# Performance work log

Hardware: AMD Instinct MI355X
Metric: run time of the kernel (lower is better)

## Reference

```python
import jax, jax.numpy as jnp
import numpy as np
import math

B, T, C = 32768, 32, 32  # seq len and embed dim are pinned to 32 by the source code


def setup_inputs() -> dict:
    key = jax.random.key(0)
    ks = jax.random.split(key, 9)
    s = 1.0 / math.sqrt(C)
    x = jax.random.normal(ks[0], (B, T, C), jnp.float32)
    Wk = jax.random.normal(ks[1], (C, C), jnp.float32) * s
    bk = jax.random.normal(ks[2], (C,), jnp.float32) * s
    Wq = jax.random.normal(ks[3], (C, C), jnp.float32) * s
    bq = jax.random.normal(ks[4], (C,), jnp.float32) * s
    Wv = jax.random.normal(ks[5], (C, C), jnp.float32) * s
    bv = jax.random.normal(ks[6], (C,), jnp.float32) * s
    Wp = jax.random.normal(ks[7], (C, C), jnp.float32) * s
    bp = jax.random.normal(ks[8], (C,), jnp.float32) * s
    return {"x": x, "Wk": Wk, "bk": bk, "Wq": Wq, "bq": bq,
            "Wv": Wv, "bv": bv, "Wp": Wp, "bp": bp}


def reference(x, Wk, bk, Wq, bq, Wv, bv, Wp, bp):
    # torch Linear: y = x @ W^T + b
    k = x @ Wk.T + bk          # [B, T, C]
    q = x @ Wq.T + bq
    v = x @ Wv.T + bv
    # att = q k^T / sqrt(C)  -> [B, T, T]
    att = jnp.matmul(q, jnp.swapaxes(k, -2, -1)) / math.sqrt(C)
    # mask is [1,1,T,T]; out-of-place masked_fill broadcasts att to [1,B,T,T]
    mask = jnp.tril(jnp.ones((T, T), jnp.float32))[None, None]  # [1,1,T,T]
    att = jnp.where(mask == 0, -jnp.inf, att[None])             # [1,B,T,T]
    att = jax.nn.softmax(att, axis=-1)
    # y = att @ v^T : [1,B,T,T] @ [B,C,T] -> [1,B,T,T]  (valid because C == T)
    y = jnp.matmul(att, jnp.swapaxes(v, -2, -1))
    # transpose(1,2) then view(B, -1, C) -- faithful permutation + reshape
    y = jnp.transpose(y, (0, 2, 1, 3)).reshape(B, -1, C)        # [B, T, C]
    return y @ Wp.T + bp
```

## Files before the change

### kernel.cpp

```cpp
#include <hip/hip_runtime.h>

typedef __bf16 bf16x8 __attribute__((ext_vector_type(8)));
typedef float  f32x16 __attribute__((ext_vector_type(16)));

static_assert(sizeof(bf16x8) == 16, "bf16x8 must be 16B");

#define MFMA32(A, B, C) __builtin_amdgcn_mfma_f32_32x32x16_bf16((A), (B), (C), 0, 0, 0)

__device__ __forceinline__ bf16x8 load8_bf(const float* __restrict__ p, float scale) {
    const float4 a = *reinterpret_cast<const float4*>(p);
    const float4 b = *reinterpret_cast<const float4*>(p + 4);
    bf16x8 r;
    r[0] = (__bf16)(a.x * scale); r[1] = (__bf16)(a.y * scale);
    r[2] = (__bf16)(a.z * scale); r[3] = (__bf16)(a.w * scale);
    r[4] = (__bf16)(b.x * scale); r[5] = (__bf16)(b.y * scale);
    r[6] = (__bf16)(b.z * scale); r[7] = (__bf16)(b.w * scale);
    return r;
}

__device__ __forceinline__ unsigned short f2bf(float f) {
    return __builtin_bit_cast(unsigned short, (__bf16)f);
}

__device__ __forceinline__ f32x16 zero16() {
    f32x16 z;
#pragma unroll
    for (int e = 0; e < 16; ++e) z[e] = 0.f;
    return z;
}


__global__ __launch_bounds__(256) void attn32(
    const float* __restrict__ x,
    const float* __restrict__ Wk, const float* __restrict__ bk,
    const float* __restrict__ Wq, const float* __restrict__ bq,
    const float* __restrict__ Wv, const float* __restrict__ bv,
    const float* __restrict__ Wp, const float* __restrict__ bp,
    float* __restrict__ out, int Btot)
{
    __shared__ float4 lds4[4][480];

    const int lane = threadIdx.x & 63;
    const int wave = threadIdx.x >> 6;
    const int col  = lane & 31;
    const int hi   = lane >> 5;

    char* const base = (char*)lds4[wave];
    unsigned short* const qk16 = (unsigned short*)base;
    unsigned short* const v16  = (unsigned short*)(base + 5120);

    const float RS32 = 0.17677669529663687f;

    const int wrow = col * 32 + hi * 8;
    const bf16x8 wk0 = load8_bf(Wk + wrow, 1.f), wk1 = load8_bf(Wk + wrow + 16, 1.f);
    const bf16x8 wq0 = load8_bf(Wq + wrow, RS32), wq1 = load8_bf(Wq + wrow + 16, RS32);
    const bf16x8 wv0 = load8_bf(Wv + wrow, 1.f), wv1 = load8_bf(Wv + wrow + 16, 1.f);
    const bf16x8 wp0 = load8_bf(Wp + wrow, 1.f), wp1 = load8_bf(Wp + wrow + 16, 1.f);
    const float bkv = bk[col];
    const float bqv = bq[col] * RS32;
    const float bvv = bv[col];
    const float bpv = bp[col];

    const int gw = blockIdx.x * (blockDim.x >> 6) + wave;
    const int nw = gridDim.x * (blockDim.x >> 6);

    for (int b = gw; b < Btot; b += nw) {
        const float* xb = x + (size_t)b * 1024;

        const bf16x8 xa0 = load8_bf(xb + col * 32 + hi * 8, 1.f);
        const bf16x8 xa1 = load8_bf(xb + col * 32 + 16 + hi * 8, 1.f);

        f32x16 acc;

        acc = zero16();
        acc = MFMA32(xa0, wk0, acc);
        acc = MFMA32(xa1, wk1, acc);
#pragma unroll
        for (int e = 0; e < 16; ++e) {
            const int r = (e & 3) + 8 * (e >> 2) + 4 * hi;
            qk16[1280 + r * 40 + col] = f2bf(acc[e] + bkv);
        }
        acc = zero16();
        acc = MFMA32(xa0, wq0, acc);
        acc = MFMA32(xa1, wq1, acc);
#pragma unroll
        for (int e = 0; e < 16; ++e) {
            const int r = (e & 3) + 8 * (e >> 2) + 4 * hi;
            qk16[r * 40 + col] = f2bf(acc[e] + bqv);
        }
        acc = zero16();
        acc = MFMA32(xa0, wv0, acc);
        acc = MFMA32(xa1, wv1, acc);
#pragma unroll
        for (int e = 0; e < 16; ++e) {
            const int r = (e & 3) + 8 * (e >> 2) + 4 * hi;
            v16[r * 40 + col] = f2bf(acc[e] + bvv);
        }

        asm volatile("" ::: "memory");

        const bf16x8 qa0 = *(const bf16x8*)(base + col * 80 + hi * 16);
        const bf16x8 qa1 = *(const bf16x8*)(base + col * 80 + 32 + hi * 16);
        const bf16x8 kb0 = *(const bf16x8*)(base + 2560 + col * 80 + hi * 16);
        const bf16x8 kb1 = *(const bf16x8*)(base + 2560 + col * 80 + 32 + hi * 16);
        acc = zero16();
        acc = MFMA32(qa0, kb0, acc);
        acc = MFMA32(qa1, kb1, acc);

        float* const sf = (float*)base;
#pragma unroll
        for (int e = 0; e < 16; ++e) {
            const int r = (e & 3) + 8 * (e >> 2) + 4 * hi;
            sf[r * 36 + col] = acc[e];
        }

        asm volatile("" ::: "memory");

        float sv[16];
        {
            const char* sb = base + col * 144 + hi * 32;
            *(float4*)&sv[0]  = *(const float4*)(sb);
            *(float4*)&sv[4]  = *(const float4*)(sb + 16);
            *(float4*)&sv[8]  = *(const float4*)(sb + 64);
            *(float4*)&sv[12] = *(const float4*)(sb + 80);
        }
        const int i = col;
#pragma unroll
        for (int e = 0; e < 16; ++e) {
            const int j = (e < 8) ? (hi * 8 + e) : (16 + hi * 8 + (e - 8));
            if (j > i) sv[e] = -__builtin_inff();
        }
        float m = sv[0];
#pragma unroll
        for (int e = 1; e < 16; ++e) m = fmaxf(m, sv[e]);
        m = fmaxf(m, __shfl_xor(m, 32));
        float pe[16];
        float sum = 0.f;
#pragma unroll
        for (int e = 0; e < 16; ++e) { pe[e] = __expf(sv[e] - m); sum += pe[e]; }
        sum += __shfl_xor(sum, 32);
        const float inv = 1.f / sum;
        bf16x8 p0, p1;
#pragma unroll
        for (int e = 0; e < 8; ++e) {
            p0[e] = (__bf16)(pe[e] * inv);
            p1[e] = (__bf16)(pe[8 + e] * inv);
        }

        const bf16x8 vb0 = *(const bf16x8*)(base + 5120 + col * 80 + hi * 16);
        const bf16x8 vb1 = *(const bf16x8*)(base + 5120 + col * 80 + 32 + hi * 16);
        acc = zero16();
        acc = MFMA32(p0, vb0, acc);
        acc = MFMA32(p1, vb1, acc);

#pragma unroll
        for (int e = 0; e < 16; ++e) {
            const int r = (e & 3) + 8 * (e >> 2) + 4 * hi;
            qk16[r * 40 + col] = f2bf(acc[e]);
        }

        asm volatile("" ::: "memory");

        const bf16x8 ya0 = *(const bf16x8*)(base + col * 80 + hi * 16);
        const bf16x8 ya1 = *(const bf16x8*)(base + col * 80 + 32 + hi * 16);
        acc = zero16();
        acc = MFMA32(ya0, wp0, acc);
        acc = MFMA32(ya1, wp1, acc);

        float* const ob = out + (size_t)b * 32 + col;
#pragma unroll
        for (int e = 0; e < 16; ++e) {
            const int r = (e & 3) + 8 * (e >> 2) + 4 * hi;
            ob[(size_t)r << 20] = acc[e] + bpv;
        }

        asm volatile("" ::: "memory");
    }
}

extern "C" void kernel_launch(void* const* d_in, const int* in_sizes, int n_in,
                              void* d_out, int out_size, void* d_ws, size_t ws_size,
                              hipStream_t stream) {
    const float* x  = (const float*)d_in[0];
    const float* Wk = (const float*)d_in[1];
    const float* bk = (const float*)d_in[2];
    const float* Wq = (const float*)d_in[3];
    const float* bq = (const float*)d_in[4];
    const float* Wv = (const float*)d_in[5];
    const float* bv = (const float*)d_in[6];
    const float* Wp = (const float*)d_in[7];
    const float* bp = (const float*)d_in[8];
    float* out = (float*)d_out;

    const int Btot = in_sizes[0] / 1024;
    dim3 grid(2048), block(256);
    hipLaunchKernelGGL(attn32, grid, block, 0, stream,
                       x, Wk, bk, Wq, bq, Wv, bv, Wp, bp, out, Btot);
}
```

Before: 60.42 us.

## Keep attention intermediates in registers via permlane32 swaps instead of LDS

Computes transposed products (W·x^T, K·Q^T, V·P^T) so each MFMA output can be repacked into the next MFMA's operand layout with bf16 packing and v_permlane32_swap, removing all LDS round-trips for Q, K, V, scores and Y. Biases are folded into the accumulator init, softmax uses exp2 with log2e folded into the Q scale plus a fast reciprocal, and the next batch's x is prefetched into registers. Output stores become nontemporal and launch bounds request 3 blocks per CU. This raises register pressure and relies on the permlane32_swap intrinsic or inline asm being available.

```diff
diff --git a/kernel.cpp b/kernel.cpp
--- a/kernel.cpp
+++ b/kernel.cpp
@@ -2,8 +2,7 @@
 
 typedef __bf16 bf16x8 __attribute__((ext_vector_type(8)));
 typedef float  f32x16 __attribute__((ext_vector_type(16)));
-
-static_assert(sizeof(bf16x8) == 16, "bf16x8 must be 16B");
+typedef unsigned int uint4v __attribute__((ext_vector_type(4)));
 
 #define MFMA32(A, B, C) __builtin_amdgcn_mfma_f32_32x32x16_bf16((A), (B), (C), 0, 0, 0)
 
@@ -18,19 +17,45 @@
     return r;
 }
 
-__device__ __forceinline__ unsigned short f2bf(float f) {
-    return __builtin_bit_cast(unsigned short, (__bf16)f);
+__device__ __forceinline__ unsigned pack2(float a, float b) {
+    unsigned la = (unsigned)__builtin_bit_cast(unsigned short, (__bf16)a);
+    unsigned lb = (unsigned)__builtin_bit_cast(unsigned short, (__bf16)b);
+    return la | (lb << 16);
 }
 
-__device__ __forceinline__ f32x16 zero16() {
-    f32x16 z;
-#pragma unroll
-    for (int e = 0; e < 16; ++e) z[e] = 0.f;
-    return z;
+__device__ __forceinline__ void swap32(unsigned& a, unsigned& b) {
+#if __has_builtin(__builtin_amdgcn_permlane32_swap)
+    auto r = __builtin_amdgcn_permlane32_swap(a, b, false, false);
+    a = r[0]; b = r[1];
+#else
+    asm("v_permlane32_swap_b32 %0, %1" : "+v"(a), "+v"(b));
+#endif
 }
 
+__device__ __forceinline__ void rearrange(const f32x16& a, bf16x8& f0, bf16x8& f1) {
+    unsigned D0 = pack2(a[0], a[1]),   D1 = pack2(a[2], a[3]);
+    unsigned D2 = pack2(a[4], a[5]),   D3 = pack2(a[6], a[7]);
+    unsigned D4 = pack2(a[8], a[9]),   D5 = pack2(a[10], a[11]);
+    unsigned D6 = pack2(a[12], a[13]), D7 = pack2(a[14], a[15]);
+    swap32(D0, D2); swap32(D1, D3); swap32(D4, D6); swap32(D5, D7);
+    f0 = __builtin_bit_cast(bf16x8, uint4v{D0, D1, D2, D3});
+    f1 = __builtin_bit_cast(bf16x8, uint4v{D4, D5, D6, D7});
+}
 
-__global__ __launch_bounds__(256) void attn32(
+__device__ __forceinline__ void ld4(const float* __restrict__ p,
+                                    float4& r0, float4& r1, float4& r2, float4& r3) {
+    r0 = *reinterpret_cast<const float4*>(p);
+    r1 = *reinterpret_cast<const float4*>(p + 4);
+    r2 = *reinterpret_cast<const float4*>(p + 16);
+    r3 = *reinterpret_cast<const float4*>(p + 20);
+}
+
+__device__ __forceinline__ void cvt8(const float4& a, const float4& b, bf16x8& f) {
+    f[0] = (__bf16)a.x; f[1] = (__bf16)a.y; f[2] = (__bf16)a.z; f[3] = (__bf16)a.w;
+    f[4] = (__bf16)b.x; f[5] = (__bf16)b.y; f[6] = (__bf16)b.z; f[7] = (__bf16)b.w;
+}
+
+__global__ __launch_bounds__(256, 3) void attn32(
     const float* __restrict__ x,
     const float* __restrict__ Wk, const float* __restrict__ bk,
     const float* __restrict__ Wq, const float* __restrict__ bq,
@@ -38,143 +63,103 @@
     const float* __restrict__ Wp, const float* __restrict__ bp,
     float* __restrict__ out, int Btot)
 {
-    __shared__ float4 lds4[4][480];
-
     const int lane = threadIdx.x & 63;
-    const int wave = threadIdx.x >> 6;
     const int col  = lane & 31;
     const int hi   = lane >> 5;
 
-    char* const base = (char*)lds4[wave];
-    unsigned short* const qk16 = (unsigned short*)base;
-    unsigned short* const v16  = (unsigned short*)(base + 5120);
-
-    const float RS32 = 0.17677669529663687f;
+    const float SC = 0.17677669529663687f * 1.4426950408889634f;
 
     const int wrow = col * 32 + hi * 8;
     const bf16x8 wk0 = load8_bf(Wk + wrow, 1.f), wk1 = load8_bf(Wk + wrow + 16, 1.f);
-    const bf16x8 wq0 = load8_bf(Wq + wrow, RS32), wq1 = load8_bf(Wq + wrow + 16, RS32);
+    const bf16x8 wq0 = load8_bf(Wq + wrow, SC),  wq1 = load8_bf(Wq + wrow + 16, SC);
     const bf16x8 wv0 = load8_bf(Wv + wrow, 1.f), wv1 = load8_bf(Wv + wrow + 16, 1.f);
     const bf16x8 wp0 = load8_bf(Wp + wrow, 1.f), wp1 = load8_bf(Wp + wrow + 16, 1.f);
-    const float bkv = bk[col];
-    const float bqv = bq[col] * RS32;
-    const float bvv = bv[col];
+
+    f32x16 bk16, bq16, bv16;
+#pragma unroll
+    for (int e = 0; e < 16; ++e) {
+        const int r = (e & 3) + 8 * (e >> 2) + 4 * hi;
+        bk16[e] = bk[r];
+        bq16[e] = bq[r] * SC;
+        bv16[e] = bv[r];
+    }
     const float bpv = bp[col];
 
-    const int gw = blockIdx.x * (blockDim.x >> 6) + wave;
-    const int nw = gridDim.x * (blockDim.x >> 6);
+    const int gw = blockIdx.x * 4 + (threadIdx.x >> 6);
+    const int nw = gridDim.x * 4;
+
+    float4 A0, A1, A2, A3;
+    if (gw < Btot) ld4(x + (size_t)gw * 1024 + wrow, A0, A1, A2, A3);
 
     for (int b = gw; b < Btot; b += nw) {
-        const float* xb = x + (size_t)b * 1024;
-
-        const bf16x8 xa0 = load8_bf(xb + col * 32 + hi * 8, 1.f);
-        const bf16x8 xa1 = load8_bf(xb + col * 32 + 16 + hi * 8, 1.f);
+        bf16x8 xa0, xa1;
+        cvt8(A0, A1, xa0);
+        cvt8(A2, A3, xa1);
+        const int nb = b + nw;
+        if (nb < Btot) ld4(x + (size_t)nb * 1024 + wrow, A0, A1, A2, A3);
 
         f32x16 acc;
 
-        acc = zero16();
-        acc = MFMA32(xa0, wk0, acc);
-        acc = MFMA32(xa1, wk1, acc);
+        acc = bk16;
+        acc = MFMA32(wk0, xa0, acc);
+        acc = MFMA32(wk1, xa1, acc);
+        bf16x8 ka0, ka1; rearrange(acc, ka0, ka1);
+
+        acc = bq16;
+        acc = MFMA32(wq0, xa0, acc);
+        acc = MFMA32(wq1, xa1, acc);
+        bf16x8 qb0, qb1; rearrange(acc, qb0, qb1);
+
+        acc = bv16;
+        acc = MFMA32(wv0, xa0, acc);
+        acc = MFMA32(wv1, xa1, acc);
+        bf16x8 vb0, vb1; rearrange(acc, vb0, vb1);
+
+        f32x16 s;
+#pragma unroll
+        for (int e = 0; e < 16; ++e) s[e] = 0.f;
+        s = MFMA32(ka0, qb0, s);
+        s = MFMA32(ka1, qb1, s);
+
+        float sv[16];
+        float m = -3.0e38f;
 #pragma unroll
         for (int e = 0; e < 16; ++e) {
-            const int r = (e & 3) + 8 * (e >> 2) + 4 * hi;
-            qk16[1280 + r * 40 + col] = f2bf(acc[e] + bkv);
+            const int j = (e & 3) + 8 * (e >> 2) + 4 * hi;
+            sv[e] = (j <= col) ? s[e] : -__builtin_inff();
+            m = fmaxf(m, sv[e]);
         }
-        acc = zero16();
-        acc = MFMA32(xa0, wq0, acc);
-        acc = MFMA32(xa1, wq1, acc);
-#pragma unroll
-        for (int e = 0; e < 16; ++e) {
-            const int r = (e & 3) + 8 * (e >> 2) + 4 * hi;
-            qk16[r * 40 + col] = f2bf(acc[e] + bqv);
-        }
-        acc = zero16();
-        acc = MFMA32(xa0, wv0, acc);
-        acc = MFMA32(xa1, wv1, acc);
-#pragma unroll
-        for (int e = 0; e < 16; ++e) {
-            const int r = (e & 3) + 8 * (e >> 2) + 4 * hi;
-            v16[r * 40 + col] = f2bf(acc[e] + bvv);
-        }
-
-        asm volatile("" ::: "memory");
-
-        const bf16x8 qa0 = *(const bf16x8*)(base + col * 80 + hi * 16);
-        const bf16x8 qa1 = *(const bf16x8*)(base + col * 80 + 32 + hi * 16);
-        const bf16x8 kb0 = *(const bf16x8*)(base + 2560 + col * 80 + hi * 16);
-        const bf16x8 kb1 = *(const bf16x8*)(base + 2560 + col * 80 + 32 + hi * 16);
-        acc = zero16();
-        acc = MFMA32(qa0, kb0, acc);
-        acc = MFMA32(qa1, kb1, acc);
-
-        float* const sf = (float*)base;
-#pragma unroll
-        for (int e = 0; e < 16; ++e) {
-            const int r = (e & 3) + 8 * (e >> 2) + 4 * hi;
-            sf[r * 36 + col] = acc[e];
-        }
-
-        asm volatile("" ::: "memory");
-
-        float sv[16];
-        {
-            const char* sb = base + col * 144 + hi * 32;
-            *(float4*)&sv[0]  = *(const float4*)(sb);
-            *(float4*)&sv[4]  = *(const float4*)(sb + 16);
-            *(float4*)&sv[8]  = *(const float4*)(sb + 64);
-            *(float4*)&sv[12] = *(const float4*)(sb + 80);
-        }
-        const int i = col;
-#pragma unroll
-        for (int e = 0; e < 16; ++e) {
-            const int j = (e < 8) ? (hi * 8 + e) : (16 + hi * 8 + (e - 8));
-            if (j > i) sv[e] = -__builtin_inff();
-        }
-        float m = sv[0];
-#pragma unroll
-        for (int e = 1; e < 16; ++e) m = fmaxf(m, sv[e]);
         m = fmaxf(m, __shfl_xor(m, 32));
         float pe[16];
         float sum = 0.f;
 #pragma unroll
-        for (int e = 0; e < 16; ++e) { pe[e] = __expf(sv[e] - m); sum += pe[e]; }
+        for (int e = 0; e < 16; ++e) { pe[e] = __builtin_amdgcn_exp2f(sv[e] - m); sum += pe[e]; }
         sum += __shfl_xor(sum, 32);
-        const float inv = 1.f / sum;
-        bf16x8 p0, p1;
+        const float inv = __builtin_amdgcn_rcpf(sum);
+        f32x16 pv;
 #pragma unroll
-        for (int e = 0; e < 8; ++e) {
-            p0[e] = (__bf16)(pe[e] * inv);
-            p1[e] = (__bf16)(pe[8 + e] * inv);
-        }
+        for (int e = 0; e < 16; ++e) pv[e] = pe[e] * inv;
+        bf16x8 pa0, pa1; rearrange(pv, pa0, pa1);
 
-        const bf16x8 vb0 = *(const bf16x8*)(base + 5120 + col * 80 + hi * 16);
-        const bf16x8 vb1 = *(const bf16x8*)(base + 5120 + col * 80 + 32 + hi * 16);
-        acc = zero16();
-        acc = MFMA32(p0, vb0, acc);
-        acc = MFMA32(p1, vb1, acc);
+        f32x16 yt;
+#pragma unroll
+        for (int e = 0; e < 16; ++e) yt[e] = 0.f;
+        yt = MFMA32(vb0, pa0, yt);
+        yt = MFMA32(vb1, pa1, yt);
+        bf16x8 ya0, ya1; rearrange(yt, ya0, ya1);
 
+        f32x16 o;
+#pragma unroll
+        for (int e = 0; e < 16; ++e) o[e] = bpv;
+        o = MFMA32(ya0, wp0, o);
+        o = MFMA32(ya1, wp1, o);
+
+        float* ob = out + (size_t)b * 32 + col;
 #pragma unroll
         for (int e = 0; e < 16; ++e) {
             const int r = (e & 3) + 8 * (e >> 2) + 4 * hi;
-            qk16[r * 40 + col] = f2bf(acc[e]);
+            __builtin_nontemporal_store(o[e], ob + ((size_t)r << 20));
         }
-
-        asm volatile("" ::: "memory");
-
-        const bf16x8 ya0 = *(const bf16x8*)(base + col * 80 + hi * 16);
-        const bf16x8 ya1 = *(const bf16x8*)(base + col * 80 + 32 + hi * 16);
-        acc = zero16();
-        acc = MFMA32(ya0, wp0, acc);
-        acc = MFMA32(ya1, wp1, acc);
-
-        float* const ob = out + (size_t)b * 32 + col;
-#pragma unroll
-        for (int e = 0; e < 16; ++e) {
-            const int r = (e & 3) + 8 * (e >> 2) + 4 * hi;
-            ob[(size_t)r << 20] = acc[e] + bpv;
-        }
-
-        asm volatile("" ::: "memory");
     }
 }
 
```

Measured after the change: 53.17 us. 12.0% less time.
